# Performance work log

Hardware: AMD Instinct MI355X
Metric: run time of the kernel (lower is better)

Reference implementation:

```python
import jax, jax.numpy as jnp
import numpy as np

NU, NT, E, H = 100000, 200000, 1000000, 64
NUM_LAYERS = 3


def setup_inputs() -> dict:
    key = jax.random.key(0)
    ks = jax.random.split(key, 16)
    s = 0.05
    inp = {}
    inp["x_user"] = jax.random.normal(ks[0], (NU, 32), jnp.float32)
    inp["x_transaction"] = jax.random.normal(ks[1], (NT, 64), jnp.float32)
    inp["ei_u2u"] = jax.random.randint(ks[2], (2, E), 0, NU, jnp.int32)
    inp["ei_t2t"] = jax.random.randint(ks[3], (2, E), 0, NT, jnp.int32)
    inp["ei_u2t"] = jnp.stack([jax.random.randint(ks[4], (E,), 0, NU),
                               jax.random.randint(ks[5], (E,), 0, NT)]).astype(jnp.int32)
    inp["ei_t2u"] = jnp.stack([jax.random.randint(ks[6], (E,), 0, NT),
                               jax.random.randint(ks[7], (E,), 0, NU)]).astype(jnp.int32)
    inp["W_emb_user"] = jax.random.normal(ks[8], (32, H), jnp.float32) * s
    inp["b_emb_user"] = jnp.zeros((H,), jnp.float32)
    inp["W_emb_txn"] = jax.random.normal(ks[9], (64, H), jnp.float32) * s
    inp["b_emb_txn"] = jnp.zeros((H,), jnp.float32)
    # one GCNConv weight/bias per (layer, edge_type): order u2u, t2t, u2t, t2u
    inp["conv_W"] = jax.random.normal(ks[10], (NUM_LAYERS, 4, H, H), jnp.float32) * s
    inp["conv_b"] = jnp.zeros((NUM_LAYERS, 4, H), jnp.float32)
    inp["W1"] = jax.random.normal(ks[11], (H, H), jnp.float32) * s
    inp["b1"] = jnp.zeros((H,), jnp.float32)
    inp["W2"] = jax.random.normal(ks[12], (H, 1), jnp.float32) * s
    inp["b2"] = jnp.zeros((1,), jnp.float32)
    return inp


def _gcn(h_src, ei, n_src, n_dst, W, b, self_loops):
    """GCNConv: x W with symmetric degree normalization, scatter-sum into dst."""
    src, dst = ei[0], ei[1]
    if self_loops:  # same node type on both ends: add self loops (PyG default)
        loop = jnp.arange(n_dst, dtype=src.dtype)
        src = jnp.concatenate([src, loop])
        dst = jnp.concatenate([dst, loop])
        deg = jax.ops.segment_sum(jnp.ones_like(dst, jnp.float32), dst, num_segments=n_dst)
        dinv = jnp.where(deg > 0, jax.lax.rsqrt(jnp.maximum(deg, 1.0)), 0.0)
        norm = dinv[src] * dinv[dst]
    else:  # bipartite relation: out-degree of src, in-degree of dst
        ds = jax.ops.segment_sum(jnp.ones_like(src, jnp.float32), src, num_segments=n_src)
        dd = jax.ops.segment_sum(jnp.ones_like(dst, jnp.float32), dst, num_segments=n_dst)
        dsi = jnp.where(ds > 0, jax.lax.rsqrt(jnp.maximum(ds, 1.0)), 0.0)
        ddi = jnp.where(dd > 0, jax.lax.rsqrt(jnp.maximum(dd, 1.0)), 0.0)
        norm = dsi[src] * ddi[dst]
    m = h_src @ W  # [N_src, H] transform first (GCNConv order)
    out = jax.ops.segment_sum(m[src] * norm[:, None], dst, num_segments=n_dst)
    return out + b


def reference(x_user, x_transaction, ei_u2u, ei_t2t, ei_u2t, ei_t2u,
              W_emb_user, b_emb_user, W_emb_txn, b_emb_txn,
              conv_W, conv_b, W1, b1, W2, b2):
    hu = x_user @ W_emb_user + b_emb_user          # [NU, H]
    ht = x_transaction @ W_emb_txn + b_emb_txn     # [NT, H]
    for l in range(NUM_LAYERS):
        ou1 = _gcn(hu, ei_u2u, NU, NU, conv_W[l, 0], conv_b[l, 0], True)
        ot1 = _gcn(ht, ei_t2t, NT, NT, conv_W[l, 1], conv_b[l, 1], True)
        ot2 = _gcn(hu, ei_u2t, NU, NT, conv_W[l, 2], conv_b[l, 2], False)
        ou2 = _gcn(ht, ei_t2u, NT, NU, conv_W[l, 3], conv_b[l, 3], False)
        # HeteroConv aggr='mean' across relations per dst type, then ReLU
        hu = jax.nn.relu((ou1 + ou2) * 0.5)
        ht = jax.nn.relu((ot1 + ot2) * 0.5)
    g = jnp.stack([hu.mean(axis=0), ht.mean(axis=0)])  # [2, H] per-type global mean
    x = g.mean(axis=0, keepdims=True)                  # [1, H]
    x = jax.nn.relu(x @ W1 + b1)                       # dropout is identity at eval
    return jax.nn.sigmoid(x @ W2 + b2)                 # [1, 1]
```

## Files before the change

### kernel.cpp

```cpp
#include <hip/hip_runtime.h>
#include <hip/hip_bf16.h>
#include <hip/hip_fp8.h>

#define NU_ 100000
#define NT_ 200000
#define NE_ 1000000
#define HD  64
#define NL  3

#define OFF0 0
#define OFF1 (NU_)
#define OFF4 (2 * NU_ + 2 * NT_)
#define OFF5 (3 * NU_ + 2 * NT_)
#define HTOT (3 * NU_ + 3 * NT_)
#define RPT2 (NU_ + NT_)

#define PB1  512
#define BKP  2048
#define NBKC 147
#define NBKS 147
#define NBKT (NBKC + NBKS)

#define WPK_EMBU 0
#define WPK_EMBT 2048
#define WPK_CONV 6144
#define WPK_G0U  55296
#define WPK_G0T  59392
#define WPK_TOT  67584
#define PK_ELEMS (WPK_TOT + 256)
#define PKB      ((PK_ELEMS + 255) / 256)

#define GMU 512
#define GMT 1024
#define GBU 3125
#define GBT 6250

typedef float floatx2 __attribute__((ext_vector_type(2)));
typedef _Float16 f16x8 __attribute__((ext_vector_type(8)));
typedef float f32x4 __attribute__((ext_vector_type(4)));
typedef unsigned short u16x8 __attribute__((ext_vector_type(8)));

__device__ __forceinline__ unsigned char enc_fp8(float v) {
    return (unsigned char)__hip_cvt_float_to_fp8(v, __HIP_SATFINITE, __HIP_E4M3);
}

__device__ __forceinline__ float dec1_fp8(unsigned int u) {
    int e = (u >> 3) & 15;
    int m = u & 7;
    int mant = m | (e ? 8 : 0);
    if (u & 0x80) mant = -mant;
    int ex = (e ? e : 1) - 10;
    return (float)mant * __uint_as_float((unsigned int)(ex + 127) << 23);
}

__device__ __forceinline__ void dec4_fp8(unsigned int u, float* f) {
#if __has_builtin(__builtin_amdgcn_cvt_pk_f32_fp8)
    floatx2 lo = __builtin_amdgcn_cvt_pk_f32_fp8((int)u, false);
    floatx2 hi = __builtin_amdgcn_cvt_pk_f32_fp8((int)u, true);
    f[0] = lo.x; f[1] = lo.y; f[2] = hi.x; f[3] = hi.y;
#else
    f[0] = dec1_fp8(u & 0xff);
    f[1] = dec1_fp8((u >> 8) & 0xff);
    f[2] = dec1_fp8((u >> 16) & 0xff);
    f[3] = dec1_fp8((u >> 24) & 0xff);
#endif
}

__global__ void detect_dtype(const unsigned short* __restrict__ x, int* __restrict__ flag, int n) {
    __shared__ int s_big;
    if (threadIdx.x == 0) s_big = 0;
    __syncthreads();
    int big = 0;
    for (int i = threadIdx.x; i < n; i += blockDim.x) {
        float v = __uint_as_float(((unsigned int)x[i]) << 16);
        if (!(fabsf(v) < 1.0e4f)) big = 1;
    }
    if (big) atomicAdd(&s_big, 1);
    __syncthreads();
    if (threadIdx.x == 0) flag[0] = (s_big > 0) ? 0 : 1;
}

struct Ptr10 { const void* p[10]; };

__global__ void cvt_weights(Ptr10 src, float* __restrict__ dst, float* __restrict__ gsum,
                            int* __restrict__ gcnt, const int* __restrict__ flag) {
    const int c[11] = {0, 2048, 2112, 6208, 6272, 55424, 56192, 60288, 60352, 60416, 60417};
    int i = blockIdx.x * blockDim.x + threadIdx.x;
    if (i < 64) gsum[i] = 0.f;
    if (i < NBKT) gcnt[i] = 0;
    if (i >= 60417) return;
    int r = 0;
#pragma unroll
    for (int k = 1; k < 10; ++k)
        if (i >= c[k]) r = k;
    int e = i - c[r];
    if (flag[0]) {
        unsigned short u = ((const unsigned short*)src.p[r])[e];
        dst[i] = __uint_as_float(((unsigned int)u) << 16);
    } else {
        dst[i] = ((const float*)src.p[r])[e];
    }
}

__device__ __forceinline__ void pack_dev(int gid, const float* __restrict__ wts,
                                         _Float16* __restrict__ wpk,
                                         float* __restrict__ bcomp) {
    if (gid >= PK_ELEMS) return;
    if (gid < WPK_G0U) {
        const float* W;
        int r, KS;
        if (gid < WPK_EMBT) { W = wts; r = gid; KS = 1; }
        else if (gid < WPK_CONV) { W = wts + 2112; r = gid - WPK_EMBT; KS = 2; }
        else {
            int mat = (gid - WPK_CONV) >> 12;
            W = wts + 6272 + mat * 4096;
            r = (gid - WPK_CONV) & 4095;
            KS = 2;
        }
        int j = r & 7;
        int lane = (r >> 3) & 63;
        int f = r >> 9;
        int ct = f / KS;
        int s = f - ct * KS;
        int k = 32 * s + 8 * (lane >> 4) + j;
        int n = 16 * ct + (lane & 15);
        wpk[gid] = (_Float16)W[k * 64 + n];
    } else if (gid < WPK_TOT) {
        const float* We;
        int matc, rr, KS;
        if (gid < WPK_G0T) {
            int r = gid - WPK_G0U;
            matc = (r >> 11) ? 2 : 0;
            rr = r & 2047;
            We = wts;
            KS = 1;
        } else {
            int r = gid - WPK_G0T;
            matc = (r >> 12) ? 3 : 1;
            rr = r & 4095;
            We = wts + 2112;
            KS = 2;
        }
        const float* Wc = wts + 6272 + matc * 4096;
        int j = rr & 7;
        int lane = (rr >> 3) & 63;
        int f = rr >> 9;
        int ct = f / KS;
        int s = f - ct * KS;
        int k = 32 * s + 8 * (lane >> 4) + j;
        int n = 16 * ct + (lane & 15);
        float acc = 0.f;
#pragma unroll
        for (int q = 0; q < 64; ++q)
            acc = fmaf(We[k * 64 + q], Wc[q * 64 + n], acc);
        wpk[gid] = (_Float16)acc;
    } else {
        int q = gid - WPK_TOT;
        int mat = q >> 6;
        int n = q & 63;
        const float* be = (mat == 0 || mat == 2) ? (wts + 2048) : (wts + 6208);
        const float* Wc = wts + 6272 + mat * 4096;
        float acc = 0.f;
#pragma unroll
        for (int k = 0; k < 64; ++k)
            acc = fmaf(be[k], Wc[k * 64 + n], acc);
        bcomp[q] = acc;
    }
}

__device__ __forceinline__ void p1_dev(int bid, const int* __restrict__ eu2u,
                                       const int* __restrict__ et2t,
                                       const int* __restrict__ eu2t,
                                       const int* __restrict__ et2u,
                                       int* __restrict__ gcnt, int* __restrict__ bofs) {
    __shared__ int cnt[NBKT];
    for (int j = threadIdx.x; j < NBKT; j += 256) cnt[j] = 0;
    __syncthreads();
    for (int i = bid * 256 + threadIdx.x; i < 6 * NE_; i += PB1 * 256) {
        int b;
        if (i < 4 * NE_) {
            int m;
            if (i < NE_)          m = eu2u[i + NE_];
            else if (i < 2 * NE_) m = NU_ + et2t[i];
            else if (i < 3 * NE_) m = NU_ + eu2t[i - NE_];
            else                  m = et2u[i - 2 * NE_];
            b = m >> 11;
        } else {
            int m2 = (i < 5 * NE_) ? eu2t[i - 4 * NE_] : (NU_ + et2u[i - 5 * NE_]);
            b = NBKC + (m2 >> 11);
        }
        atomicAdd(&cnt[b], 1);
    }
    __syncthreads();
    for (int j = threadIdx.x; j < NBKT; j += 256) {
        bofs[bid * NBKT + j] = atomicAdd(&gcnt[j], cnt[j]);
    }
}

__global__ __launch_bounds__(256) void fused_p1_pack(
    const int* __restrict__ eu2u, const int* __restrict__ et2t,
    const int* __restrict__ eu2t, const int* __restrict__ et2u,
    int* __restrict__ gcnt, int* __restrict__ bofs,
    const float* __restrict__ wts, _Float16* __restrict__ wpk, float* __restrict__ bcomp) {
    int b = blockIdx.x;
    if (b < PB1) {
        p1_dev(b, eu2u, et2t, eu2t, et2u, gcnt, bofs);
    } else {
        pack_dev((b - PB1) * 256 + threadIdx.x, wts, wpk, bcomp);
    }
}

__global__ __launch_bounds__(256) void p2_scatter(
    const int* __restrict__ eu2u, const int* __restrict__ et2t,
    const int* __restrict__ eu2t, const int* __restrict__ et2u,
    const int* __restrict__ gcnt, int* __restrict__ gbase, const int* __restrict__ bofs,
    unsigned int* __restrict__ part_csr, unsigned int* __restrict__ part_src) {
    __shared__ int gb[NBKT];
    __shared__ int lofs[NBKT];
    const int t = threadIdx.x;
    for (int j = t; j < NBKT; j += 256) { lofs[j] = 0; gb[j] = gcnt[j]; }
    __syncthreads();
    if (t == 0) {
        int s = 0;
        for (int j = 0; j < NBKC; ++j) { int c = gb[j]; gb[j] = s; s += c; }
        s = 0;
        for (int j = NBKC; j < NBKT; ++j) { int c = gb[j]; gb[j] = s; s += c; }
    }
    __syncthreads();
    const int bid = blockIdx.x;
    if (bid == 0)
        for (int j = t; j < NBKT; j += 256) gbase[j] = gb[j];
    for (int i = bid * 256 + t; i < 6 * NE_; i += PB1 * 256) {
        if (i < 4 * NE_) {
            int m; unsigned int src, tag;
            if (i < NE_)          { m = eu2u[i + NE_];        src = (unsigned int)eu2u[i];           tag = 0u; }
            else if (i < 2 * NE_) { m = NU_ + et2t[i];        src = (unsigned int)et2t[i - NE_];     tag = 0u; }
            else if (i < 3 * NE_) { m = NU_ + eu2t[i - NE_];  src = (unsigned int)eu2t[i - 2 * NE_]; tag = 1u; }
            else                  { m = et2u[i - 2 * NE_];    src = (unsigned int)et2u[i - 3 * NE_]; tag = 1u; }
            int b = m >> 11;
            int l = atomicAdd(&lofs[b], 1);
            int pos = gb[b] + bofs[bid * NBKT + b] + l;
            part_csr[pos] = (src << 12) | (tag << 11) | (unsigned int)(m & (BKP - 1));
        } else {
            int m2 = (i < 5 * NE_) ? eu2t[i - 4 * NE_] : (NU_ + et2u[i - 5 * NE_]);
            int b = NBKC + (m2 >> 11);
            int l = atomicAdd(&lofs[b], 1);
            int pos = gb[b] + bofs[bid * NBKT + b] + l;
            part_src[pos] = (unsigned int)m2;
        }
    }
}

__global__ __launch_bounds__(1024) void bucket_build(
    const unsigned int* __restrict__ part_csr, const unsigned int* __restrict__ part_src,
    const int* __restrict__ gcnt, const int* __restrict__ gbase,
    float* __restrict__ dinv, int4* __restrict__ meta,
    int* __restrict__ colU, int* __restrict__ colT) {
    const int b = blockIdx.x;
    const int t = threadIdx.x;
    if (b >= NBKC) {
        __shared__ int cS[BKP];
        const int n = gcnt[b];
        const int base = gbase[b];
        for (int j = t; j < BKP; j += 1024) cS[j] = 0;
        __syncthreads();
        for (int i = t; i < n; i += 1024)
            atomicAdd(&cS[(int)(part_src[base + i] & (BKP - 1))], 1);
        __syncthreads();
        const int m0 = (b - NBKC) << 11;
        for (int j = t; j < BKP; j += 1024) {
            int m2 = m0 + j;
            if (m2 < NU_ + NT_) {
                int o = (m2 < NU_) ? (OFF4 + m2) : (OFF5 + (m2 - NU_));
                int h = cS[j];
                dinv[o] = (h > 0) ? rsqrtf((float)h) : 0.f;
            }
        }
        return;
    }
    __shared__ int cA[BKP];
    __shared__ int cB[BKP];
    __shared__ int lp[BKP];
    __shared__ int s1[1024];
    const int n = gcnt[b];
    const int base = gbase[b];
    for (int j = t; j < BKP; j += 1024) { cA[j] = 0; cB[j] = 0; }
    __syncthreads();
    for (int i = t; i < n; i += 1024) {
        unsigned int it = part_csr[base + i];
        int l = (int)(it & (BKP - 1));
        if (it & 0x800u) atomicAdd(&cB[l], 1);
        else             atomicAdd(&cA[l], 1);
    }
    __syncthreads();
    const int j0 = t << 1, j1 = j0 + 1;
    const int a0 = cA[j0] + cB[j0];
    const int a1 = cA[j1] + cB[j1];
    const int ps = a0 + a1;
    s1[t] = ps;
    __syncthreads();
    for (int off = 1; off < 1024; off <<= 1) {
        int x = (t >= off) ? s1[t - off] : 0;
        __syncthreads();
        s1[t] += x;
        __syncthreads();
    }
    const int excl = s1[t] - ps;
    lp[j0] = excl;
    lp[j1] = excl + a0;
    __syncthreads();
    const int m0 = b << 11;
    const int gb0 = gbase[b];
    for (int j = t; j < BKP; j += 1024) {
        int m = m0 + j;
        if (m < NU_ + NT_) {
            int hA = cA[j], hB = cB[j];
            float dslf = rsqrtf((float)hA + 1.0f);
            int oA = (m < NU_) ? (OFF0 + m) : (OFF1 + (m - NU_));
            dinv[oA] = dslf;
            int4 mt;
            mt.x = gb0 + lp[j] - ((m >= NU_) ? 2 * NE_ : 0);
            mt.y = hA + hB;
            mt.z = __float_as_int(0.5f * dslf);
            mt.w = __float_as_int((hB > 0) ? 0.5f * rsqrtf((float)hB) : 0.f);
            meta[m] = mt;
        }
    }
    __syncthreads();
    for (int j = t; j < BKP; j += 1024) cA[j] = 0;
    __syncthreads();
    for (int i = t; i < n; i += 1024) {
        unsigned int it = part_csr[base + i];
        int mlow = (int)(it & (BKP - 1));
        int ofs = atomicAdd(&cA[mlow], 1);
        int g = gb0 + lp[mlow] + ofs;
        int colv = (int)(((it >> 12) << 6) | ((it & 0x800u) << 20));
        int m = m0 + mlow;
        if (m < NU_) colU[g] = colv;
        else         colT[g - 2 * NE_] = colv;
    }
}

template <int K>
__device__ __forceinline__ void gemm0_dev(int t0, int tstride, int ntiles,
                                          const void* __restrict__ x,
                                          const _Float16* __restrict__ WApk,
                                          const _Float16* __restrict__ WBpk,
                                          const float* __restrict__ bA,
                                          const float* __restrict__ bB,
                                          const float* __restrict__ scA,
                                          const float* __restrict__ scB,
                                          unsigned char* __restrict__ mA,
                                          unsigned char* __restrict__ mB,
                                          const int* __restrict__ flag) {
    constexpr int KS = K / 32;
    const int lane = threadIdx.x & 63;
    const int rq = lane & 15;
    const int oct = lane >> 4;

    f16x8 bf[2][4][KS];
#pragma unroll
    for (int m = 0; m < 2; ++m) {
        const _Float16* P = m ? WBpk : WApk;
#pragma unroll
        for (int ct = 0; ct < 4; ++ct)
#pragma unroll
            for (int s = 0; s < KS; ++s)
                bf[m][ct][s] = *(const f16x8*)(P + (((ct * KS + s) << 9) + (lane << 3)));
    }
    float bvA[4], bvB[4];
#pragma unroll
    for (int ct = 0; ct < 4; ++ct) { bvA[ct] = bA[16 * ct + rq]; bvB[ct] = bB[16 * ct + rq]; }

    const bool isb = flag[0] != 0;

    for (int t = t0; t < ntiles; t += tstride) {
        const int r0 = t << 4;
        f16x8 a[KS];
        if (isb) {
            const unsigned short* xr = (const unsigned short*)x + (size_t)(r0 + rq) * K + 8 * oct;
#pragma unroll
            for (int s = 0; s < KS; ++s) {
                u16x8 uv = *(const u16x8*)(xr + 32 * s);
                f16x8 v;
#pragma unroll
                for (int j = 0; j < 8; ++j)
                    v[j] = (_Float16)__uint_as_float(((unsigned int)uv[j]) << 16);
                a[s] = v;
            }
        } else {
            const float* xr = (const float*)x + (size_t)(r0 + rq) * K + 8 * oct;
#pragma unroll
            for (int s = 0; s < KS; ++s) {
                float4 x0 = *(const float4*)(xr + 32 * s);
                float4 x1 = *(const float4*)(xr + 32 * s + 4);
                f16x8 v;
                v[0] = (_Float16)x0.x; v[1] = (_Float16)x0.y;
                v[2] = (_Float16)x0.z; v[3] = (_Float16)x0.w;
                v[4] = (_Float16)x1.x; v[5] = (_Float16)x1.y;
                v[6] = (_Float16)x1.z; v[7] = (_Float16)x1.w;
                a[s] = v;
            }
        }

        f32x4 acc[2][4];
#pragma unroll
        for (int m = 0; m < 2; ++m)
#pragma unroll
            for (int ct = 0; ct < 4; ++ct) acc[m][ct] = (f32x4){0.f, 0.f, 0.f, 0.f};
#pragma unroll
        for (int m = 0; m < 2; ++m)
#pragma unroll
            for (int ct = 0; ct < 4; ++ct)
#pragma unroll
                for (int s = 0; s < KS; ++s)
                    acc[m][ct] = __builtin_amdgcn_mfma_f32_16x16x32_f16(a[s], bf[m][ct][s],
                                                                       acc[m][ct], 0, 0, 0);

        const int rb = r0 + (oct << 2);
        float sa[4], sb[4];
#pragma unroll
        for (int g = 0; g < 4; ++g) { sa[g] = scA[rb + g]; sb[g] = scB[rb + g]; }
#pragma unroll
        for (int ct = 0; ct < 4; ++ct)
#pragma unroll
            for (int g = 0; g < 4; ++g) {
                mA[(size_t)(rb + g) * HD + 16 * ct + rq] =
                    enc_fp8((acc[0][ct][g] + bvA[ct]) * sa[g]);
                mB[(size_t)(rb + g) * HD + 16 * ct + rq] =
                    enc_fp8((acc[1][ct][g] + bvB[ct]) * sb[g]);
            }
    }
}

__global__ __launch_bounds__(256) void gemm0_both(
    const void* __restrict__ x_user, const void* __restrict__ x_txn,
    const _Float16* __restrict__ wpk, const float* __restrict__ bcomp,
    const float* __restrict__ dinv,
    unsigned char* __restrict__ m_uu, unsigned char* __restrict__ m_ut,
    unsigned char* __restrict__ m_tt, unsigned char* __restrict__ m_tu,
    const int* __restrict__ flag) {
    int b = blockIdx.x;
    int wid = threadIdx.x >> 6;
    if (b < GMU) {
        gemm0_dev<32>(b * 4 + wid, GMU * 4, NU_ / 16, x_user,
                      wpk + WPK_G0U, wpk + WPK_G0U + 2048,
                      bcomp + 0, bcomp + 128,
                      dinv + OFF0, dinv + OFF4, m_uu, m_ut, flag);
    } else {
        gemm0_dev<64>((b - GMU) * 4 + wid, GMT * 4, NT_ / 16, x_txn,
                      wpk + WPK_G0T, wpk + WPK_G0T + 4096,
                      bcomp + 64, bcomp + 192,
                      dinv + OFF1, dinv + OFF5, m_tt, m_tu, flag);
    }
}

__device__ __forceinline__ void gather_phase(int d, bool valid,
                                             const unsigned char* __restrict__ msg,
                                             unsigned int offB,
                                             const int4* __restrict__ meta,
                                             const int* __restrict__ col,
                                             const float* __restrict__ ba,
                                             const float* __restrict__ bb,
                                             float* __restrict__ af) {
    const int lane = threadIdx.x & 63;
    const int grp = lane >> 3;
    const int sub = lane & 7;

    int4 mt = make_int4(0, 0, 0, 0);
    if (valid) mt = meta[d];
    const int st = mt.x;
    const int cnt = mt.y;
    const float dA = __int_as_float(mt.z);
    const float dB = __int_as_float(mt.w);
    const unsigned char* msgL = msg + (sub << 3);

    floatx2 acc[4];
#pragma unroll
    for (int q = 0; q < 4; ++q) acc[q] = (floatx2){0.f, 0.f};

    auto consume = [&](uint2 u, float s) {
        floatx2 s2; s2.x = s; s2.y = s;
#if __has_builtin(__builtin_amdgcn_cvt_pk_f32_fp8)
        acc[0] += __builtin_amdgcn_cvt_pk_f32_fp8((int)u.x, false) * s2;
        acc[1] += __builtin_amdgcn_cvt_pk_f32_fp8((int)u.x, true) * s2;
        acc[2] += __builtin_amdgcn_cvt_pk_f32_fp8((int)u.y, false) * s2;
        acc[3] += __builtin_amdgcn_cvt_pk_f32_fp8((int)u.y, true) * s2;
#else
        float f[8];
        dec4_fp8(u.x, f);
        dec4_fp8(u.y, f + 4);
        acc[0].x += f[0] * s; acc[0].y += f[1] * s;
        acc[1].x += f[2] * s; acc[1].y += f[3] * s;
        acc[2].x += f[4] * s; acc[2].y += f[5] * s;
        acc[3].x += f[6] * s; acc[3].y += f[7] * s;
#endif
    };

    if (valid) {
        uint2 uself = *(const uint2*)(msgL + ((unsigned int)d << 6));
        consume(uself, dA);
    }

    int cw = (sub < cnt) ? col[st + sub] : 0;
    int done = 0;
    while (done < cnt) {
        int rem = cnt - done;
        if (rem > 8) rem = 8;

        uint2 ub0, ub1, ub2, ub3, ub4, ub5, ub6, ub7;
        float sc0, sc1, sc2, sc3, sc4, sc5, sc6, sc7;

        auto issue = [&](int p, uint2& ub, float& sc) {
            int c = __shfl(cw, (grp << 3) + p);
            unsigned int off = ((unsigned int)c & 0x7fffffffu) + ((c < 0) ? offB : 0u);
            sc = (p < rem) ? ((c < 0) ? dB : dA) : 0.f;
            ub = *(const uint2*)(msgL + off);
        };

        issue(0, ub0, sc0);
        issue(1, ub1, sc1);
        issue(2, ub2, sc2);
        issue(3, ub3, sc3);
        issue(4, ub4, sc4);
        issue(5, ub5, sc5);
        issue(6, ub6, sc6);
        issue(7, ub7, sc7);

        int nd = done + 8;
        int cw2 = (nd + sub < cnt) ? col[st + nd + sub] : 0;

        consume(ub0, sc0);
        consume(ub1, sc1);
        consume(ub2, sc2);
        consume(ub3, sc3);
        consume(ub4, sc4);
        consume(ub5, sc5);
        consume(ub6, sc6);
        consume(ub7, sc7);

        cw = cw2;
        done = nd;
    }

    const int col0 = sub << 3;
    float4 a0 = *(const float4*)(ba + col0);
    float4 a1 = *(const float4*)(ba + col0 + 4);
    float4 c0 = *(const float4*)(bb + col0);
    float4 c1 = *(const float4*)(bb + col0 + 4);
    float av[8] = {acc[0].x, acc[0].y, acc[1].x, acc[1].y,
                   acc[2].x, acc[2].y, acc[3].x, acc[3].y};
    float bv[8] = {a0.x + c0.x, a0.y + c0.y, a0.z + c0.z, a0.w + c0.w,
                   a1.x + c1.x, a1.y + c1.y, a1.z + c1.z, a1.w + c1.w};
#pragma unroll
    for (int k = 0; k < 8; ++k)
        af[k] = fmaxf(av[k] + 0.5f * bv[k], 0.f);
}

__global__ __launch_bounds__(256) void gather_red_both(
    const unsigned char* __restrict__ msgU, const unsigned char* __restrict__ msgT,
    const int4* __restrict__ meta,
    const int* __restrict__ colU, const int* __restrict__ colT,
    const float* __restrict__ bU0, const float* __restrict__ bU1,
    const float* __restrict__ bT0, const float* __restrict__ bT1,
    float* __restrict__ partU, float* __restrict__ partT) {
    __shared__ float hs[32][64];
    __shared__ float ps[4][64];
    int b = blockIdx.x;
    const bool isU = b < GBU;
    const int blk = isU ? b : b - GBU;
    const int grp = (threadIdx.x & 63) >> 3;
    const int sub = threadIdx.x & 7;
    const int w = threadIdx.x >> 6;
    const int d = (blk << 5) + (w << 3) + grp;
    const int N = isU ? NU_ : NT_;
    float af[8];
    gather_phase(d, d < N,
                 isU ? msgU : msgT, (unsigned int)(isU ? NU_ : NT_) * HD,
                 isU ? meta : meta + NU_, isU ? colU : colT,
                 isU ? bU0 : bT0, isU ? bU1 : bT1, af);
    {
        const int ld = threadIdx.x >> 3;
#pragma unroll
        for (int k = 0; k < 8; ++k) hs[ld][(sub << 3) + k] = (d < N) ? af[k] : 0.f;
    }
    __syncthreads();
    const int c = threadIdx.x & 63;
    const int r0 = w << 3;
    float s = 0.f;
#pragma unroll
    for (int r = 0; r < 8; ++r) s += hs[r0 + r][c];
    ps[w][c] = s;
    __syncthreads();
    if (threadIdx.x < 64) {
        float t = ps[0][c] + ps[1][c] + ps[2][c] + ps[3][c];
        (isU ? partU : partT)[(size_t)blk * 64 + c] = t;
    }
}

__global__ __launch_bounds__(256) void gather_gemm_both(
    const unsigned char* __restrict__ msgU, const unsigned char* __restrict__ msgT,
    const int4* __restrict__ meta,
    const int* __restrict__ colU, const int* __restrict__ colT,
    const float* __restrict__ bU0, const float* __restrict__ bU1,
    const float* __restrict__ bT0, const float* __restrict__ bT1,
    const _Float16* __restrict__ WUa, const _Float16* __restrict__ WUb,
    const _Float16* __restrict__ WTa, const _Float16* __restrict__ WTb,
    const float* __restrict__ dinv,
    unsigned char* __restrict__ o_uu, unsigned char* __restrict__ o_ut,
    unsigned char* __restrict__ o_tt, unsigned char* __restrict__ o_tu) {
    __shared__ _Float16 hs[32][64];
    int b = blockIdx.x;
    const bool isU = b < GBU;
    const int blk = isU ? b : b - GBU;
    const int lane = threadIdx.x & 63;
    const int grp = lane >> 3;
    const int sub = lane & 7;
    const int w = threadIdx.x >> 6;
    const int d = (blk << 5) + (w << 3) + grp;
    const int N = isU ? NU_ : NT_;

    float af[8];
    gather_phase(d, d < N,
                 isU ? msgU : msgT, (unsigned int)(isU ? NU_ : NT_) * HD,
                 isU ? meta : meta + NU_, isU ? colU : colT,
                 isU ? bU0 : bT0, isU ? bU1 : bT1, af);

    {
        const int ld = threadIdx.x >> 3;
        f16x8 o;
#pragma unroll
        for (int k = 0; k < 8; ++k) o[k] = (_Float16)af[k];
        *(f16x8*)(&hs[ld][sub << 3]) = o;
    }
    __syncthreads();

    {
        const int half = w & 1;
        const int mi = w >> 1;
        const _Float16* P = mi ? (isU ? WUb : WTb) : (isU ? WUa : WTa);
        unsigned char* mOut = mi ? (isU ? o_ut : o_tu) : (isU ? o_uu : o_tt);
        const float* sc = dinv + (mi ? (isU ? OFF4 : OFF5) : (isU ? OFF0 : OFF1));
        const int rq = lane & 15;
        const int oct = lane >> 4;

        f16x8 bf[4][2];
#pragma unroll
        for (int ct = 0; ct < 4; ++ct)
#pragma unroll
            for (int s = 0; s < 2; ++s)
                bf[ct][s] = *(const f16x8*)(P + ((((ct << 1) + s) << 9) + (lane << 3)));

        f16x8 a0 = *(const f16x8*)(&hs[16 * half + rq][8 * oct]);
        f16x8 a1 = *(const f16x8*)(&hs[16 * half + rq][32 + 8 * oct]);

        f32x4 acc[4];
#pragma unroll
        for (int ct = 0; ct < 4; ++ct) acc[ct] = (f32x4){0.f, 0.f, 0.f, 0.f};
#pragma unroll
        for (int ct = 0; ct < 4; ++ct) {
            acc[ct] = __builtin_amdgcn_mfma_f32_16x16x32_f16(a0, bf[ct][0], acc[ct], 0, 0, 0);
            acc[ct] = __builtin_amdgcn_mfma_f32_16x16x32_f16(a1, bf[ct][1], acc[ct], 0, 0, 0);
        }

        const int rb = (blk << 5) + 16 * half + (oct << 2);
        float sv[4];
#pragma unroll
        for (int g = 0; g < 4; ++g) sv[g] = sc[rb + g];
#pragma unroll
        for (int ct = 0; ct < 4; ++ct)
#pragma unroll
            for (int g = 0; g < 4; ++g)
                mOut[(size_t)(rb + g) * HD + 16 * ct + rq] = enc_fp8(acc[ct][g] * sv[g]);
    }
}

__global__ __launch_bounds__(256) void colmean_small(const float* __restrict__ partU,
                                                     const float* __restrict__ partT,
                                                     float* __restrict__ gsum) {
    const bool isU = blockIdx.x < 8;
    const float* p = isU ? partU : partT;
    const int rows = isU ? GBU : GBT;
    const float scale = isU ? 0.5f / NU_ : 0.5f / NT_;
    const int blk = isU ? blockIdx.x : blockIdx.x - 8;
    const int lane = threadIdx.x & 63;
    const int wv = threadIdx.x >> 6;
    float s = 0.f;
    for (int r = blk * 4 + wv; r < rows; r += 32)
        s += p[(size_t)r * 64 + lane];
    __shared__ float red[256];
    red[threadIdx.x] = s;
    __syncthreads();
    if (threadIdx.x < 64) {
        float t = red[threadIdx.x] + red[64 + threadIdx.x] + red[128 + threadIdx.x] +
                  red[192 + threadIdx.x];
        atomicAdd(&gsum[lane], t * scale);
    }
}

__global__ void head(const float* __restrict__ g, const float* __restrict__ W1,
                     const float* __restrict__ b1, const float* __restrict__ W2,
                     const float* __restrict__ b2, const int* __restrict__ flag,
                     void* __restrict__ out) {
    const int c = threadIdx.x;
    float x = b1[c];
    for (int k = 0; k < HD; ++k) x = fmaf(g[k], W1[k * HD + c], x);
    x = fmaxf(x, 0.f);
    float t = x * W2[c];
    for (int off = 32; off; off >>= 1) t += __shfl_down(t, off);
    if (c == 0) {
        float z = t + b2[0];
        float s = 1.f / (1.f + expf(-z));
        if (flag[0]) *(__hip_bfloat16*)out = __float2bfloat16(s);
        else *(float*)out = s;
    }
}

extern "C" void kernel_launch(void* const* d_in, const int* in_sizes, int n_in,
                              void* d_out, int out_size, void* d_ws, size_t ws_size,
                              hipStream_t stream) {
    const void* x_user = d_in[0];
    const void* x_txn  = d_in[1];
    const int* ei_u2u = (const int*)d_in[2];
    const int* ei_t2t = (const int*)d_in[3];
    const int* ei_u2t = (const int*)d_in[4];
    const int* ei_t2u = (const int*)d_in[5];

    float* ws = (float*)d_ws;
    float* partU = ws;
    float* partT = partU + (size_t)GBU * 64;
    float* dinv = (float*)((_Float16*)ws + (size_t)RPT2 * HD);
    float* wts = dinv + HTOT;
    float* gsum = wts + 60432;
    float* bcomp = gsum + 64;
    _Float16* wpk = (_Float16*)(bcomp + 256);
    unsigned char* msg0 = (unsigned char*)(wpk + WPK_TOT);
    unsigned char* msg1 = msg0 + (size_t)(2 * NU_ + 2 * NT_) * HD;
    int* aux  = (int*)(msg1 + (size_t)(2 * NU_ + 2 * NT_) * HD);
    int* colU = aux + 2 * NBKT + PB1 * NBKT;
    int* colT = colU + 2 * NE_;
    int4* meta = (int4*)(colT + 2 * NE_);
    int* dflag = (int*)(meta + RPT2);

    int* gcnt  = aux;
    int* gbase = gcnt + NBKT;
    int* bofs  = gbase + NBKT;

    auto uu = [](unsigned char* s) { return s; };
    auto tu = [](unsigned char* s) { return s + (size_t)NU_ * HD; };
    auto tt = [](unsigned char* s) { return s + (size_t)(NU_ + NT_) * HD; };
    auto ut = [](unsigned char* s) { return s + (size_t)(NU_ + 2 * NT_) * HD; };

    unsigned int* part_csr = (unsigned int*)msg1;
    unsigned int* part_src = (unsigned int*)ws;

    float* W1f = wts + 56192;
    float* b1f = W1f + 4096;
    float* W2f = b1f + 64;
    float* b2f = W2f + 64;
    const float* convbf = wts + 55424;

    detect_dtype<<<1, 256, 0, stream>>>((const unsigned short*)x_user, dflag, 2048);
    {
        Ptr10 p;
        for (int k = 0; k < 10; ++k) p.p[k] = d_in[6 + k];
        cvt_weights<<<(60417 + 255) / 256, 256, 0, stream>>>(p, wts, gsum, gcnt, dflag);
    }

    fused_p1_pack<<<PB1 + PKB, 256, 0, stream>>>(ei_u2u, ei_t2t, ei_u2t, ei_t2u,
                                                 gcnt, bofs, wts, wpk, bcomp);

    p2_scatter<<<PB1, 256, 0, stream>>>(ei_u2u, ei_t2t, ei_u2t, ei_t2u,
                                        gcnt, gbase, bofs, part_csr, part_src);

    bucket_build<<<NBKT, 1024, 0, stream>>>(part_csr, part_src, gcnt, gbase,
                                            dinv, meta, colU, colT);

    gemm0_both<<<GMU + GMT, 256, 0, stream>>>(x_user, x_txn, wpk, bcomp, dinv,
                                              uu(msg0), ut(msg0), tt(msg0), tu(msg0), dflag);

    for (int l = 0; l < 2; ++l) {
        unsigned char* in  = (l == 0) ? msg0 : msg1;
        unsigned char* out = (l == 0) ? msg1 : msg0;
        const float* B0   = convbf + ((size_t)l * 4 + 0) * HD;
        const float* Bt   = convbf + ((size_t)l * 4 + 1) * HD;
        const float* Bu2t = convbf + ((size_t)l * 4 + 2) * HD;
        const float* Bt2u = convbf + ((size_t)l * 4 + 3) * HD;
        const _Float16* W0n   = wpk + WPK_CONV + ((size_t)(l + 1) * 4 + 0) * 4096;
        const _Float16* Wtn   = wpk + WPK_CONV + ((size_t)(l + 1) * 4 + 1) * 4096;
        const _Float16* Wu2tn = wpk + WPK_CONV + ((size_t)(l + 1) * 4 + 2) * 4096;
        const _Float16* Wt2un = wpk + WPK_CONV + ((size_t)(l + 1) * 4 + 3) * 4096;

        gather_gemm_both<<<GBU + GBT, 256, 0, stream>>>(
            uu(in), tt(in), meta, colU, colT,
            B0, Bt2u, Bt, Bu2t,
            W0n, Wu2tn, Wtn, Wt2un, dinv,
            uu(out), ut(out), tt(out), tu(out));
    }

    {
        const float* B0   = convbf + (2 * 4 + 0) * HD;
        const float* Bt   = convbf + (2 * 4 + 1) * HD;
        const float* Bu2t = convbf + (2 * 4 + 2) * HD;
        const float* Bt2u = convbf + (2 * 4 + 3) * HD;
        gather_red_both<<<GBU + GBT, 256, 0, stream>>>(uu(msg0), tt(msg0),
                                                       meta, colU, colT,
                                                       B0, Bt2u, Bt, Bu2t, partU, partT);
    }

    colmean_small<<<16, 256, 0, stream>>>(partU, partT, gsum);
    head<<<1, 64, 0, stream>>>(gsum, W1f, b1f, W2f, b2f, dflag, d_out);
}
```

Measured before the change: 552.3 us.

## Fuse setup and tail kernels, merge head into colmean, use nontemporal loads

Moves the zero-initialisation of gsum and the bucket counters into detect_dtype, so weight conversion can share a launch with the edge bucket count (p1). Weight packing now shares a launch with the scatter pass (p2). colmean and head become one kernel, where the last block to finish (found with an atomic counter) computes the MLP head. Edge index, partition and CSR column loads become nontemporal. The goal is to cut kernel launches and cache pollution from streamed data, at the cost of a last-block synchronisation pattern and an extra done counter that must be reset.

After: 597.0 us. 1.08x slower.

```diff
diff --git a/kernel.cpp b/kernel.cpp
--- a/kernel.cpp
+++ b/kernel.cpp
@@ -29,6 +29,7 @@
 #define WPK_TOT  67584
 #define PK_ELEMS (WPK_TOT + 256)
 #define PKB      ((PK_ELEMS + 255) / 256)
+#define CVB      237
 
 #define GMU 512
 #define GMT 1024
@@ -39,6 +40,7 @@
 typedef _Float16 f16x8 __attribute__((ext_vector_type(8)));
 typedef float f32x4 __attribute__((ext_vector_type(4)));
 typedef unsigned short u16x8 __attribute__((ext_vector_type(8)));
+typedef int i32x4 __attribute__((ext_vector_type(4)));
 
 __device__ __forceinline__ unsigned char enc_fp8(float v) {
     return (unsigned char)__hip_cvt_float_to_fp8(v, __HIP_SATFINITE, __HIP_E4M3);
@@ -66,7 +68,9 @@
 #endif
 }
 
-__global__ void detect_dtype(const unsigned short* __restrict__ x, int* __restrict__ flag, int n) {
+__global__ void detect_dtype(const unsigned short* __restrict__ x, int* __restrict__ flag,
+                             float* __restrict__ gsum, int* __restrict__ gcnt,
+                             int* __restrict__ done, int n) {
     __shared__ int s_big;
     if (threadIdx.x == 0) s_big = 0;
     __syncthreads();
@@ -76,18 +80,18 @@
         if (!(fabsf(v) < 1.0e4f)) big = 1;
     }
     if (big) atomicAdd(&s_big, 1);
+    if (threadIdx.x < 64) gsum[threadIdx.x] = 0.f;
+    for (int j = threadIdx.x; j < NBKT; j += 256) gcnt[j] = 0;
+    if (threadIdx.x == 0) *done = 0;
     __syncthreads();
     if (threadIdx.x == 0) flag[0] = (s_big > 0) ? 0 : 1;
 }
 
 struct Ptr10 { const void* p[10]; };
 
-__global__ void cvt_weights(Ptr10 src, float* __restrict__ dst, float* __restrict__ gsum,
-                            int* __restrict__ gcnt, const int* __restrict__ flag) {
+__device__ __forceinline__ void cvt_dev(int i, Ptr10 src, float* __restrict__ dst,
+                                        const int* __restrict__ flag) {
     const int c[11] = {0, 2048, 2112, 6208, 6272, 55424, 56192, 60288, 60352, 60416, 60417};
-    int i = blockIdx.x * blockDim.x + threadIdx.x;
-    if (i < 64) gsum[i] = 0.f;
-    if (i < NBKT) gcnt[i] = 0;
     if (i >= 60417) return;
     int r = 0;
 #pragma unroll
@@ -180,13 +184,14 @@
         int b;
         if (i < 4 * NE_) {
             int m;
-            if (i < NE_)          m = eu2u[i + NE_];
-            else if (i < 2 * NE_) m = NU_ + et2t[i];
-            else if (i < 3 * NE_) m = NU_ + eu2t[i - NE_];
-            else                  m = et2u[i - 2 * NE_];
+            if (i < NE_)          m = __builtin_nontemporal_load(eu2u + i + NE_);
+            else if (i < 2 * NE_) m = NU_ + __builtin_nontemporal_load(et2t + i);
+            else if (i < 3 * NE_) m = NU_ + __builtin_nontemporal_load(eu2t + i - NE_);
+            else                  m = __builtin_nontemporal_load(et2u + i - 2 * NE_);
             b = m >> 11;
         } else {
-            int m2 = (i < 5 * NE_) ? eu2t[i - 4 * NE_] : (NU_ + et2u[i - 5 * NE_]);
+            int m2 = (i < 5 * NE_) ? __builtin_nontemporal_load(eu2t + i - 4 * NE_)
+                                   : (NU_ + __builtin_nontemporal_load(et2u + i - 5 * NE_));
             b = NBKC + (m2 >> 11);
         }
         atomicAdd(&cnt[b], 1);
@@ -197,24 +202,27 @@
     }
 }
 
-__global__ __launch_bounds__(256) void fused_p1_pack(
+__global__ __launch_bounds__(256) void fused_cvt_p1(
+    Ptr10 src, float* __restrict__ wts, const int* __restrict__ flag,
     const int* __restrict__ eu2u, const int* __restrict__ et2t,
     const int* __restrict__ eu2t, const int* __restrict__ et2u,
-    int* __restrict__ gcnt, int* __restrict__ bofs,
-    const float* __restrict__ wts, _Float16* __restrict__ wpk, float* __restrict__ bcomp) {
+    int* __restrict__ gcnt, int* __restrict__ bofs) {
     int b = blockIdx.x;
-    if (b < PB1) {
-        p1_dev(b, eu2u, et2t, eu2t, et2u, gcnt, bofs);
+    if (b < CVB) {
+        cvt_dev(b * 256 + threadIdx.x, src, wts, flag);
     } else {
-        pack_dev((b - PB1) * 256 + threadIdx.x, wts, wpk, bcomp);
-    }
-}
-
-__global__ __launch_bounds__(256) void p2_scatter(
-    const int* __restrict__ eu2u, const int* __restrict__ et2t,
-    const int* __restrict__ eu2t, const int* __restrict__ et2u,
-    const int* __restrict__ gcnt, int* __restrict__ gbase, const int* __restrict__ bofs,
-    unsigned int* __restrict__ part_csr, unsigned int* __restrict__ part_src) {
+        p1_dev(b - CVB, eu2u, et2t, eu2t, et2u, gcnt, bofs);
+    }
+}
+
+__device__ __forceinline__ void p2_dev(int bid, const int* __restrict__ eu2u,
+                                       const int* __restrict__ et2t,
+                                       const int* __restrict__ eu2t,
+                                       const int* __restrict__ et2u,
+                                       const int* __restrict__ gcnt, int* __restrict__ gbase,
+                                       const int* __restrict__ bofs,
+                                       unsigned int* __restrict__ part_csr,
+                                       unsigned int* __restrict__ part_src) {
     __shared__ int gb[NBKT];
     __shared__ int lofs[NBKT];
     const int t = threadIdx.x;
@@ -227,27 +235,45 @@
         for (int j = NBKC; j < NBKT; ++j) { int c = gb[j]; gb[j] = s; s += c; }
     }
     __syncthreads();
-    const int bid = blockIdx.x;
     if (bid == 0)
         for (int j = t; j < NBKT; j += 256) gbase[j] = gb[j];
     for (int i = bid * 256 + t; i < 6 * NE_; i += PB1 * 256) {
         if (i < 4 * NE_) {
             int m; unsigned int src, tag;
-            if (i < NE_)          { m = eu2u[i + NE_];        src = (unsigned int)eu2u[i];           tag = 0u; }
-            else if (i < 2 * NE_) { m = NU_ + et2t[i];        src = (unsigned int)et2t[i - NE_];     tag = 0u; }
-            else if (i < 3 * NE_) { m = NU_ + eu2t[i - NE_];  src = (unsigned int)eu2t[i - 2 * NE_]; tag = 1u; }
-            else                  { m = et2u[i - 2 * NE_];    src = (unsigned int)et2u[i - 3 * NE_]; tag = 1u; }
+            if (i < NE_)          { m = __builtin_nontemporal_load(eu2u + i + NE_);
+                                    src = (unsigned int)__builtin_nontemporal_load(eu2u + i);            tag = 0u; }
+            else if (i < 2 * NE_) { m = NU_ + __builtin_nontemporal_load(et2t + i);
+                                    src = (unsigned int)__builtin_nontemporal_load(et2t + i - NE_);      tag = 0u; }
+            else if (i < 3 * NE_) { m = NU_ + __builtin_nontemporal_load(eu2t + i - NE_);
+                                    src = (unsigned int)__builtin_nontemporal_load(eu2t + i - 2 * NE_);  tag = 1u; }
+            else                  { m = __builtin_nontemporal_load(et2u + i - 2 * NE_);
+                                    src = (unsigned int)__builtin_nontemporal_load(et2u + i - 3 * NE_);  tag = 1u; }
             int b = m >> 11;
             int l = atomicAdd(&lofs[b], 1);
             int pos = gb[b] + bofs[bid * NBKT + b] + l;
             part_csr[pos] = (src << 12) | (tag << 11) | (unsigned int)(m & (BKP - 1));
         } else {
-            int m2 = (i < 5 * NE_) ? eu2t[i - 4 * NE_] : (NU_ + et2u[i - 5 * NE_]);
+            int m2 = (i < 5 * NE_) ? __builtin_nontemporal_load(eu2t + i - 4 * NE_)
+                                   : (NU_ + __builtin_nontemporal_load(et2u + i - 5 * NE_));
             int b = NBKC + (m2 >> 11);
             int l = atomicAdd(&lofs[b], 1);
             int pos = gb[b] + bofs[bid * NBKT + b] + l;
             part_src[pos] = (unsigned int)m2;
         }
+    }
+}
+
+__global__ __launch_bounds__(256) void fused_pack_p2(
+    const float* __restrict__ wts, _Float16* __restrict__ wpk, float* __restrict__ bcomp,
+    const int* __restrict__ eu2u, const int* __restrict__ et2t,
+    const int* __restrict__ eu2t, const int* __restrict__ et2u,
+    const int* __restrict__ gcnt, int* __restrict__ gbase, const int* __restrict__ bofs,
+    unsigned int* __restrict__ part_csr, unsigned int* __restrict__ part_src) {
+    int b = blockIdx.x;
+    if (b < PKB) {
+        pack_dev(b * 256 + threadIdx.x, wts, wpk, bcomp);
+    } else {
+        p2_dev(b - PKB, eu2u, et2t, eu2t, et2u, gcnt, gbase, bofs, part_csr, part_src);
     }
 }
 
@@ -265,7 +291,7 @@
         for (int j = t; j < BKP; j += 1024) cS[j] = 0;
         __syncthreads();
         for (int i = t; i < n; i += 1024)
-            atomicAdd(&cS[(int)(part_src[base + i] & (BKP - 1))], 1);
+            atomicAdd(&cS[(int)(__builtin_nontemporal_load(part_src + base + i) & (BKP - 1))], 1);
         __syncthreads();
         const int m0 = (b - NBKC) << 11;
         for (int j = t; j < BKP; j += 1024) {
@@ -287,7 +313,7 @@
     for (int j = t; j < BKP; j += 1024) { cA[j] = 0; cB[j] = 0; }
     __syncthreads();
     for (int i = t; i < n; i += 1024) {
-        unsigned int it = part_csr[base + i];
+        unsigned int it = __builtin_nontemporal_load(part_csr + base + i);
         int l = (int)(it & (BKP - 1));
         if (it & 0x800u) atomicAdd(&cB[l], 1);
         else             atomicAdd(&cA[l], 1);
@@ -330,7 +356,7 @@
     for (int j = t; j < BKP; j += 1024) cA[j] = 0;
     __syncthreads();
     for (int i = t; i < n; i += 1024) {
-        unsigned int it = part_csr[base + i];
+        unsigned int it = __builtin_nontemporal_load(part_csr + base + i);
         int mlow = (int)(it & (BKP - 1));
         int ofs = atomicAdd(&cA[mlow], 1);
         int g = gb0 + lp[mlow] + ofs;
@@ -467,8 +493,8 @@
     const int grp = lane >> 3;
     const int sub = lane & 7;
 
-    int4 mt = make_int4(0, 0, 0, 0);
-    if (valid) mt = meta[d];
+    i32x4 mt = (i32x4){0, 0, 0, 0};
+    if (valid) mt = __builtin_nontemporal_load((const i32x4*)(meta + d));
     const int st = mt.x;
     const int cnt = mt.y;
     const float dA = __int_as_float(mt.z);
@@ -502,7 +528,7 @@
         consume(uself, dA);
     }
 
-    int cw = (sub < cnt) ? col[st + sub] : 0;
+    int cw = (sub < cnt) ? __builtin_nontemporal_load(col + st + sub) : 0;
     int done = 0;
     while (done < cnt) {
         int rem = cnt - done;
@@ -528,7 +554,7 @@
         issue(7, ub7, sc7);
 
         int nd = done + 8;
-        int cw2 = (nd + sub < cnt) ? col[st + nd + sub] : 0;
+        int cw2 = (nd + sub < cnt) ? __builtin_nontemporal_load(col + st + nd + sub) : 0;
 
         consume(ub0, sc0);
         consume(ub1, sc1);
@@ -675,9 +701,12 @@
     }
 }
 
-__global__ __launch_bounds__(256) void colmean_small(const float* __restrict__ partU,
-                                                     const float* __restrict__ partT,
-                                                     float* __restrict__ gsum) {
+__global__ __launch_bounds__(256) void colmean_head(
+    const float* __restrict__ partU, const float* __restrict__ partT,
+    float* __restrict__ gsum, int* __restrict__ done,
+    const float* __restrict__ W1, const float* __restrict__ b1,
+    const float* __restrict__ W2, const float* __restrict__ b2,
+    const int* __restrict__ flag, void* __restrict__ out) {
     const bool isU = blockIdx.x < 8;
     const float* p = isU ? partU : partT;
     const int rows = isU ? GBU : GBT;
@@ -689,6 +718,8 @@
     for (int r = blk * 4 + wv; r < rows; r += 32)
         s += p[(size_t)r * 64 + lane];
     __shared__ float red[256];
+    __shared__ int islast;
+    __shared__ float gsh[64];
     red[threadIdx.x] = s;
     __syncthreads();
     if (threadIdx.x < 64) {
@@ -696,23 +727,32 @@
                   red[192 + threadIdx.x];
         atomicAdd(&gsum[lane], t * scale);
     }
-}
-
-__global__ void head(const float* __restrict__ g, const float* __restrict__ W1,
-                     const float* __restrict__ b1, const float* __restrict__ W2,
-                     const float* __restrict__ b2, const int* __restrict__ flag,
-                     void* __restrict__ out) {
-    const int c = threadIdx.x;
-    float x = b1[c];
-    for (int k = 0; k < HD; ++k) x = fmaf(g[k], W1[k * HD + c], x);
-    x = fmaxf(x, 0.f);
-    float t = x * W2[c];
-    for (int off = 32; off; off >>= 1) t += __shfl_down(t, off);
-    if (c == 0) {
-        float z = t + b2[0];
-        float s = 1.f / (1.f + expf(-z));
-        if (flag[0]) *(__hip_bfloat16*)out = __float2bfloat16(s);
-        else *(float*)out = s;
+    __syncthreads();
+    if (threadIdx.x == 0) {
+        __threadfence();
+        int prev = __hip_atomic_fetch_add(done, 1, __ATOMIC_ACQ_REL, __HIP_MEMORY_SCOPE_AGENT);
+        islast = (prev == 15) ? 1 : 0;
+    }
+    __syncthreads();
+    if (islast) {
+        if (threadIdx.x < 64)
+            gsh[threadIdx.x] = __hip_atomic_load(&gsum[threadIdx.x], __ATOMIC_RELAXED,
+                                                 __HIP_MEMORY_SCOPE_AGENT);
+    }
+    __syncthreads();
+    if (islast && threadIdx.x < 64) {
+        const int c = threadIdx.x;
+        float x = b1[c];
+        for (int k = 0; k < HD; ++k) x = fmaf(gsh[k], W1[k * HD + c], x);
+        x = fmaxf(x, 0.f);
+        float t = x * W2[c];
+        for (int off = 32; off; off >>= 1) t += __shfl_down(t, off);
+        if (c == 0) {
+            float z = t + b2[0];
+            float sg = 1.f / (1.f + expf(-z));
+            if (flag[0]) *(__hip_bfloat16*)out = __float2bfloat16(sg);
+            else *(float*)out = sg;
+        }
     }
 }
 
@@ -741,6 +781,7 @@
     int* colT = colU + 2 * NE_;
     int4* meta = (int4*)(colT + 2 * NE_);
     int* dflag = (int*)(meta + RPT2);
+    int* done  = dflag + 1;
 
     int* gcnt  = aux;
     int* gbase = gcnt + NBKT;
@@ -760,18 +801,20 @@
     float* b2f = W2f + 64;
     const float* convbf = wts + 55424;
 
-    detect_dtype<<<1, 256, 0, stream>>>((const unsigned short*)x_user, dflag, 2048);
+    detect_dtype<<<1, 256, 0, stream>>>((const unsigned short*)x_user, dflag,
+                                        gsum, gcnt, done, 2048);
+
     {
         Ptr10 p;
         for (int k = 0; k < 10; ++k) p.p[k] = d_in[6 + k];
-        cvt_weights<<<(60417 + 255) / 256, 256, 0, stream>>>(p, wts, gsum, gcnt, dflag);
-    }
-
-    fused_p1_pack<<<PB1 + PKB, 256, 0, stream>>>(ei_u2u, ei_t2t, ei_u2t, ei_t2u,
-                                                 gcnt, bofs, wts, wpk, bcomp);
-
-    p2_scatter<<<PB1, 256, 0, stream>>>(ei_u2u, ei_t2t, ei_u2t, ei_t2u,
-                                        gcnt, gbase, bofs, part_csr, part_src);
+        fused_cvt_p1<<<CVB + PB1, 256, 0, stream>>>(p, wts, dflag,
+                                                    ei_u2u, ei_t2t, ei_u2t, ei_t2u,
+                                                    gcnt, bofs);
+    }
+
+    fused_pack_p2<<<PKB + PB1, 256, 0, stream>>>(wts, wpk, bcomp,
+                                                 ei_u2u, ei_t2t, ei_u2t, ei_t2u,
+                                                 gcnt, gbase, bofs, part_csr, part_src);
 
     bucket_build<<<NBKT, 1024, 0, stream>>>(part_csr, part_src, gcnt, gbase,
                                             dinv, meta, colU, colT);
@@ -808,6 +851,6 @@
                                                        B0, Bt2u, Bt, Bu2t, partU, partT);
     }
 
-    colmean_small<<<16, 256, 0, stream>>>(partU, partT, gsum);
-    head<<<1, 64, 0, stream>>>(gsum, W1f, b1f, W2f, b2f, dflag, d_out);
-}
+    colmean_head<<<16, 256, 0, stream>>>(partU, partT, gsum, done,
+                                         W1f, b1f, W2f, b2f, dflag, d_out);
+}
```
